# Optimization experiments

Measured on AMD Instinct MI355X. Metric: run time of the kernel, lower is better.

The kernel has to match this reference:

```python
import jax, jax.numpy as jnp
import numpy as np

MARGIN = 0.2
BIG = 1e9  # sentinel for masked (positive-pair) entries in the row-min


def setup_inputs() -> dict:
    key = jax.random.key(0)
    k1, k2, k3 = jax.random.split(key, 3)
    B, D, NUM_CLASSES = 4096, 512, 1000
    z_s = jax.random.normal(k1, (B, D), dtype=jnp.float32)
    z_i = jax.random.normal(k2, (B, D), dtype=jnp.float32)
    labels = jax.random.randint(k3, (B,), 0, NUM_CLASSES, dtype=jnp.int64)
    return {"z_s": z_s, "z_i": z_i, "labels": labels}


def reference(z_s, z_i, labels):
    # dists[a, b] = 1 - <z_s[a], z_i[b]>   -- [B, B]
    dists = 1.0 - jnp.einsum("ad,bd->ab", z_s, z_i)
    pos_mask = labels[:, None] == labels[None, :]  # [B, B] same-label pairs

    p = jnp.diagonal(dists)  # positive distance per anchor, [B]
    # hardest negative per anchor: min over entries with different label
    n = jnp.min(jnp.where(pos_mask, BIG, dists), axis=1)  # [B]
    has_neg = ~jnp.all(pos_mask, axis=1)  # anchors with at least one negative

    per_anchor = jax.nn.relu(p - n + MARGIN)  # [B]
    count = jnp.sum(has_neg)
    total = jnp.sum(jnp.where(has_neg, per_anchor, 0.0))
    # mean over anchors that had negatives; 0.0 if none (matches torch fallback)
    return jnp.where(count > 0, total / jnp.maximum(count, 1).astype(total.dtype), 0.0)
```

## Files before the change

### kernel.cpp

```cpp
#include <hip/hip_runtime.h>
#include <hip/hip_bf16.h>

typedef __attribute__((ext_vector_type(8))) short bf16x8;
typedef __attribute__((ext_vector_type(4))) float f32x4;

#define NB 4096
#define ND 512
#define MARGIN_F 0.2f

__device__ __forceinline__ unsigned int enc_f32(float f) {
    unsigned int b = __float_as_uint(f);
    return (b & 0x80000000u) ? ~b : (b | 0x80000000u);
}

__device__ __forceinline__ float dec_f32(unsigned int e) {
    unsigned int b = (e & 0x80000000u) ? (e & 0x7fffffffu) : ~e;
    return __uint_as_float(b);
}

__device__ __forceinline__ void gld_lds16(const void* g, void* l) {
    __builtin_amdgcn_global_load_lds((__attribute__((address_space(1))) void*)g,
                                     (__attribute__((address_space(3))) void*)l,
                                     16, 0, 0);
}

__device__ __forceinline__ float selv(f32x4 v, int r) {
    float s01 = (r & 1) ? v[1] : v[0];
    float s23 = (r & 1) ? v[3] : v[2];
    return (r & 2) ? s23 : s01;
}

__global__ __launch_bounds__(256) void k_prep(const float* __restrict__ zs,
                                              const float* __restrict__ zi,
                                              __hip_bfloat16* __restrict__ outb,
                                              unsigned int* __restrict__ rowmax) {
    const int bid = blockIdx.x;
    if (bid < 16) rowmax[bid * 256 + threadIdx.x] = 0u;

    int gid = bid * 256 + threadIdx.x;
    int mat = gid >> 18;
    int t   = gid & 0x3FFFF;
    int si  = t >> 6;
    int L   = t & 63;
    const float* src = mat ? zi : zs;
    int row = ((si >> 4) << 4) | (L & 15);
    int col = ((si & 15) << 5) | (((L >> 4) & 3) << 3);
    const float4* p = (const float4*)(src + (size_t)row * ND + col);
    float4 f0 = p[0];
    float4 f1 = p[1];
    union { __hip_bfloat16 h[8]; bf16x8 v; } u;
    u.h[0] = __float2bfloat16(f0.x);
    u.h[1] = __float2bfloat16(f0.y);
    u.h[2] = __float2bfloat16(f0.z);
    u.h[3] = __float2bfloat16(f0.w);
    u.h[4] = __float2bfloat16(f1.x);
    u.h[5] = __float2bfloat16(f1.y);
    u.h[6] = __float2bfloat16(f1.z);
    u.h[7] = __float2bfloat16(f1.w);
    bf16x8* dst = (bf16x8*)(outb + ((size_t)mat << 21) + ((size_t)si << 9) + (L << 3));
    *dst = u.v;
}

__global__ __launch_bounds__(512, 2) void k_gemm_rowmax(const __hip_bfloat16* __restrict__ zsb,
                                                        const __hip_bfloat16* __restrict__ zib,
                                                        const int* __restrict__ labels,
                                                        unsigned int* __restrict__ rowmax,
                                                        float* __restrict__ p_diag) {
    __shared__ __align__(16) unsigned char lds[131072];
    __shared__ int labA[256];
    __shared__ int labB[256];

    const int tid = threadIdx.x;
    const int bid = blockIdx.x;
    const int xcd = bid & 7, lid = bid >> 3;
    const int bx = ((xcd & 3) << 2) | (lid & 3);
    const int by = ((xcd >> 2) << 3) | (lid >> 2);

    if (tid < 256) labA[tid] = labels[by * 256 + tid];
    else           labB[tid & 255] = labels[bx * 256 + (tid & 255)];

    const char* gA = (const char*)zsb;
    const char* gB = (const char*)zib;
    const int inner = (tid & 127) << 4;
    const int aB16 = by * 16 + (tid >> 7);
    const int bB16 = bx * 16 + (tid >> 7);

#define STAGE(kt, h) do {                                                          \
        const char* _g = ((h) & 2) ? gB : gA;                                      \
        int _rb = (((h) & 2) ? bB16 : aB16) + (((h) & 1) << 3);                    \
        unsigned _ld = (((kt) & 1) << 16) + ((h) << 14) + (tid << 4);              \
        gld_lds16(_g + (((size_t)_rb) << 14) + ((kt) << 11) + inner, lds + _ld);   \
        gld_lds16(_g + (((size_t)(_rb + 4)) << 14) + ((kt) << 11) + inner,         \
                  lds + _ld + 8192);                                               \
    } while (0)

    const int w = tid >> 6, lane = tid & 63;
    const int w_m = w >> 2, w_n = w & 3;
    const unsigned fragOff = (unsigned)(lane << 4);
    const unsigned aBase = (unsigned)(w_m << 14) + fragOff;
    const unsigned bBase = 32768u + (unsigned)((w_n >> 1) << 14)
                         + (unsigned)(((w_n & 1) << 2) << 11) + fragOff;

    const f32x4 Z4 = (f32x4){0.f, 0.f, 0.f, 0.f};
    f32x4 acc00=Z4, acc01=Z4, acc02=Z4, acc03=Z4;
    f32x4 acc10=Z4, acc11=Z4, acc12=Z4, acc13=Z4;
    f32x4 acc20=Z4, acc21=Z4, acc22=Z4, acc23=Z4;
    f32x4 acc30=Z4, acc31=Z4, acc32=Z4, acc33=Z4;
    f32x4 acc40=Z4, acc41=Z4, acc42=Z4, acc43=Z4;
    f32x4 acc50=Z4, acc51=Z4, acc52=Z4, acc53=Z4;
    f32x4 acc60=Z4, acc61=Z4, acc62=Z4, acc63=Z4;
    f32x4 acc70=Z4, acc71=Z4, acc72=Z4, acc73=Z4;
    bf16x8 a_0, a_1, a_2, a_3, b_0, b_1, b_2, b_3;

#define MF(A, B, C) __builtin_amdgcn_mfma_f32_16x16x32_bf16((A), (B), (C), 0, 0, 0)
#define LDB(koff)                                                              \
    b_0 = *(const bf16x8*)(lds + par + bBase + (0 << 11) + (koff));            \
    b_1 = *(const bf16x8*)(lds + par + bBase + (1 << 11) + (koff));            \
    b_2 = *(const bf16x8*)(lds + par + bBase + (2 << 11) + (koff));            \
    b_3 = *(const bf16x8*)(lds + par + bBase + (3 << 11) + (koff));
#define LDA(mh, koff)                                                          \
    a_0 = *(const bf16x8*)(lds + par + aBase + ((((mh) << 2) + 0) << 11) + (koff)); \
    a_1 = *(const bf16x8*)(lds + par + aBase + ((((mh) << 2) + 1) << 11) + (koff)); \
    a_2 = *(const bf16x8*)(lds + par + aBase + ((((mh) << 2) + 2) << 11) + (koff)); \
    a_3 = *(const bf16x8*)(lds + par + aBase + ((((mh) << 2) + 3) << 11) + (koff));
#define ROW4(A, R)                                                             \
    acc##R##0 = MF((A), b_0, acc##R##0);                                       \
    acc##R##1 = MF((A), b_1, acc##R##1);                                       \
    acc##R##2 = MF((A), b_2, acc##R##2);                                       \
    acc##R##3 = MF((A), b_3, acc##R##3);
#define PHASE_SYNC()                                                           \
    __builtin_amdgcn_s_barrier();                                              \
    asm volatile("s_waitcnt lgkmcnt(0)" ::: "memory");                         \
    __builtin_amdgcn_sched_barrier(0);

    STAGE(0, 0); STAGE(0, 1); STAGE(0, 2); STAGE(0, 3);
    STAGE(1, 2); STAGE(1, 3);
    __syncthreads();

#pragma unroll
    for (int kt = 0; kt < 8; ++kt) {
        const unsigned par = (unsigned)((kt & 1) << 16);

        LDB(0)
        LDA(0, 0)
        if (kt < 7) STAGE(kt + 1, 0);
        PHASE_SYNC()
        __builtin_amdgcn_s_setprio(1);
        ROW4(a_0, 0) ROW4(a_1, 1) ROW4(a_2, 2) ROW4(a_3, 3)
        __builtin_amdgcn_s_setprio(0);
        __builtin_amdgcn_s_barrier();

        LDA(1, 0)
        if (kt < 7) STAGE(kt + 1, 1);
        PHASE_SYNC()
        __builtin_amdgcn_s_setprio(1);
        ROW4(a_0, 4) ROW4(a_1, 5) ROW4(a_2, 6) ROW4(a_3, 7)
        __builtin_amdgcn_s_setprio(0);
        __builtin_amdgcn_s_barrier();

        LDB(1024)
        LDA(0, 1024)
        PHASE_SYNC()
        __builtin_amdgcn_s_setprio(1);
        ROW4(a_0, 0) ROW4(a_1, 1) ROW4(a_2, 2) ROW4(a_3, 3)
        __builtin_amdgcn_s_setprio(0);
        __builtin_amdgcn_s_barrier();

        LDA(1, 1024)
        if (kt < 6) { STAGE(kt + 2, 2); STAGE(kt + 2, 3); }
        PHASE_SYNC()
        __builtin_amdgcn_s_setprio(1);
        ROW4(a_0, 4) ROW4(a_1, 5) ROW4(a_2, 6) ROW4(a_3, 7)
        __builtin_amdgcn_s_setprio(0);
        if (kt < 6) {
            asm volatile("s_waitcnt vmcnt(4)" ::: "memory");
            __builtin_amdgcn_s_barrier();
        } else if (kt == 6) {
            asm volatile("s_waitcnt vmcnt(0)" ::: "memory");
            __builtin_amdgcn_s_barrier();
        }
    }
#undef STAGE
#undef LDA
#undef LDB
#undef ROW4
#undef PHASE_SYNC

    const int quad = lane >> 4;
    const int lcol = lane & 15;
    const int epiBase = by * 256 + w_m * 128 + quad * 4;

    const int lb_0 = labB[w_n * 64 + 0 * 16 + lcol];
    const int lb_1 = labB[w_n * 64 + 1 * 16 + lcol];
    const int lb_2 = labB[w_n * 64 + 2 * 16 + lcol];
    const int lb_3 = labB[w_n * 64 + 3 * 16 + lcol];

#define EPIV(m, n, LB) {                                                       \
        float v0 = acc##m##n[0], v1 = acc##m##n[1];                            \
        float v2 = acc##m##n[2], v3 = acc##m##n[3];                            \
        if (la0 != (LB) && v0 > mx0) mx0 = v0;                                 \
        if (la1 != (LB) && v1 > mx1) mx1 = v1;                                 \
        if (la2 != (LB) && v2 > mx2) mx2 = v2;                                 \
        if (la3 != (LB) && v3 > mx3) mx3 = v3; }
#define EPIRED(m, r, MX) {                                                     \
        float mm = (MX);                                                       \
        mm = fmaxf(mm, __shfl_xor(mm, 1));                                     \
        mm = fmaxf(mm, __shfl_xor(mm, 2));                                     \
        mm = fmaxf(mm, __shfl_xor(mm, 4));                                     \
        mm = fmaxf(mm, __shfl_xor(mm, 8));                                     \
        if (lcol == 0 && mm > -2.9e38f)                                        \
            atomicMax(&rowmax[epiBase + (m) * 16 + (r)], enc_f32(mm)); }
#define EPIMS(m) {                                                             \
        int la0 = labA[w_m * 128 + (m) * 16 + quad * 4 + 0];                   \
        int la1 = labA[w_m * 128 + (m) * 16 + quad * 4 + 1];                   \
        int la2 = labA[w_m * 128 + (m) * 16 + quad * 4 + 2];                   \
        int la3 = labA[w_m * 128 + (m) * 16 + quad * 4 + 3];                   \
        float mx0 = -3.0e38f, mx1 = -3.0e38f, mx2 = -3.0e38f, mx3 = -3.0e38f;  \
        EPIV(m, 0, lb_0) EPIV(m, 1, lb_1) EPIV(m, 2, lb_2) EPIV(m, 3, lb_3)    \
        EPIRED(m, 0, mx0) EPIRED(m, 1, mx1) EPIRED(m, 2, mx2) EPIRED(m, 3, mx3) }

    EPIMS(0) EPIMS(1) EPIMS(2) EPIMS(3)
    EPIMS(4) EPIMS(5) EPIMS(6) EPIMS(7)
#undef EPIMS
#undef EPIRED
#undef EPIV

    if (bx == by && (w_n >> 1) == w_m && (lcol >> 2) == quad) {
        int r = lcol & 3;
        f32x4 d0 = (w_n & 1) ? acc40 : acc00;
        f32x4 d1 = (w_n & 1) ? acc51 : acc11;
        f32x4 d2 = (w_n & 1) ? acc62 : acc22;
        f32x4 d3 = (w_n & 1) ? acc73 : acc33;
        int base = by * 256 + w_m * 128 + ((w_n & 1) << 6) + lcol;
        p_diag[base +  0] = 1.0f - selv(d0, r);
        p_diag[base + 16] = 1.0f - selv(d1, r);
        p_diag[base + 32] = 1.0f - selv(d2, r);
        p_diag[base + 48] = 1.0f - selv(d3, r);
    }
}

__global__ __launch_bounds__(1024) void k_finalize(const unsigned int* __restrict__ rowmax,
                                                   const float* __restrict__ p_diag,
                                                   float* __restrict__ out) {
    int tid = threadIdx.x;
    float sum = 0.0f;
    int cnt = 0;
#pragma unroll
    for (int it = 0; it < 4; ++it) {
        int a = tid + it * 1024;
        unsigned int e = rowmax[a];
        if (e != 0u) {
            float n = 1.0f - dec_f32(e);
            float per = p_diag[a] - n + MARGIN_F;
            if (per > 0.0f) sum += per;
            cnt++;
        }
    }
#pragma unroll
    for (int off = 32; off > 0; off >>= 1) {
        sum += __shfl_xor(sum, off);
        cnt += __shfl_xor(cnt, off);
    }
    __shared__ float sSum[16];
    __shared__ int sCnt[16];
    int w = tid >> 6, lane = tid & 63;
    if (lane == 0) { sSum[w] = sum; sCnt[w] = cnt; }
    __syncthreads();
    if (tid == 0) {
        float ts = 0.0f;
        int tc = 0;
#pragma unroll
        for (int i = 0; i < 16; ++i) { ts += sSum[i]; tc += sCnt[i]; }
        out[0] = (tc > 0) ? ts / (float)tc : 0.0f;
    }
}

extern "C" void kernel_launch(void* const* d_in, const int* in_sizes, int n_in,
                              void* d_out, int out_size, void* d_ws, size_t ws_size,
                              hipStream_t stream) {
    (void)in_sizes; (void)n_in; (void)out_size; (void)ws_size;
    const float* zs = (const float*)d_in[0];
    const float* zi = (const float*)d_in[1];
    const int* labels = (const int*)d_in[2];
    float* out = (float*)d_out;

    char* ws = (char*)d_ws;
    __hip_bfloat16* zb = (__hip_bfloat16*)ws;
    unsigned int* rowmax = (unsigned int*)(ws + (8u << 20));
    float* p_diag = (float*)(ws + (8u << 20) + 16384);

    k_prep<<<2048, 256, 0, stream>>>(zs, zi, zb, rowmax);
    k_gemm_rowmax<<<256, 512, 0, stream>>>(zb, zb + (size_t)NB * ND, labels, rowmax, p_diag);
    k_finalize<<<1, 1024, 0, stream>>>(rowmax, p_diag, out);
}
```

Measured before the change: 97.80 us.

## Restructure LDS staging into k-half quarters with per-phase A/B loads

Changes the global-to-LDS staging so each stage loads both A and B for a half k-slice (1 KB columns per row) instead of splitting A and B loads across phases, and adjusts the LDS fragment addressing to match the new layout. The prefetch schedule now issues the next k-tile's two halves in the first and third phases, with vmcnt waits inserted after the second and fourth phases. The goal is to even out the memory traffic across the compute phases and shorten the prologue. The trade-off is that the wait points and dependencies change, which can expose load latency if the prefetch distance is now shorter.

```diff
diff --git a/kernel.cpp b/kernel.cpp
--- a/kernel.cpp
+++ b/kernel.cpp
@@ -77,29 +77,29 @@
     const int by = ((xcd >> 2) << 3) | (lid >> 2);
 
     if (tid < 256) labA[tid] = labels[by * 256 + tid];
-    else           labB[tid & 255] = labels[bx * 256 + (tid & 255)];
+    else           labB[tid & 255] = labels[bx * 256 + (tid - 256)];
 
     const char* gA = (const char*)zsb;
     const char* gB = (const char*)zib;
-    const int inner = (tid & 127) << 4;
-    const int aB16 = by * 16 + (tid >> 7);
-    const int bB16 = bx * 16 + (tid >> 7);
-
-#define STAGE(kt, h) do {                                                          \
-        const char* _g = ((h) & 2) ? gB : gA;                                      \
-        int _rb = (((h) & 2) ? bB16 : aB16) + (((h) & 1) << 3);                    \
-        unsigned _ld = (((kt) & 1) << 16) + ((h) << 14) + (tid << 4);              \
-        gld_lds16(_g + (((size_t)_rb) << 14) + ((kt) << 11) + inner, lds + _ld);   \
-        gld_lds16(_g + (((size_t)(_rb + 4)) << 14) + ((kt) << 11) + inner,         \
-                  lds + _ld + 8192);                                               \
+    const int rbw = tid >> 6;
+    const int cw  = (tid & 63) << 4;
+    const int aQ = by * 16;
+    const int bQ = bx * 16;
+
+#define STAGEQ(kt, q) do {                                                         \
+        size_t _gc = ((size_t)((((kt) << 1) | (q)) << 10)) + cw;                   \
+        unsigned _ld = (((kt) & 1) << 16) + ((q) << 14) + (tid << 4);              \
+        gld_lds16(gA + (((size_t)(aQ + rbw))     << 14) + _gc, lds + _ld);         \
+        gld_lds16(gA + (((size_t)(aQ + 8 + rbw)) << 14) + _gc, lds + _ld + 8192);  \
+        gld_lds16(gB + (((size_t)(bQ + rbw))     << 14) + _gc, lds + _ld + 32768); \
+        gld_lds16(gB + (((size_t)(bQ + 8 + rbw)) << 14) + _gc, lds + _ld + 40960); \
     } while (0)
 
     const int w = tid >> 6, lane = tid & 63;
     const int w_m = w >> 2, w_n = w & 3;
     const unsigned fragOff = (unsigned)(lane << 4);
-    const unsigned aBase = (unsigned)(w_m << 14) + fragOff;
-    const unsigned bBase = 32768u + (unsigned)((w_n >> 1) << 14)
-                         + (unsigned)(((w_n & 1) << 2) << 11) + fragOff;
+    const unsigned aBase2 = (unsigned)(w_m << 13) + fragOff;
+    const unsigned bBase2 = 32768u + (unsigned)(w_n << 12) + fragOff;
 
     const f32x4 Z4 = (f32x4){0.f, 0.f, 0.f, 0.f};
     f32x4 acc00=Z4, acc01=Z4, acc02=Z4, acc03=Z4;
@@ -113,16 +113,16 @@
     bf16x8 a_0, a_1, a_2, a_3, b_0, b_1, b_2, b_3;
 
 #define MF(A, B, C) __builtin_amdgcn_mfma_f32_16x16x32_bf16((A), (B), (C), 0, 0, 0)
-#define LDB(koff)                                                              \
-    b_0 = *(const bf16x8*)(lds + par + bBase + (0 << 11) + (koff));            \
-    b_1 = *(const bf16x8*)(lds + par + bBase + (1 << 11) + (koff));            \
-    b_2 = *(const bf16x8*)(lds + par + bBase + (2 << 11) + (koff));            \
-    b_3 = *(const bf16x8*)(lds + par + bBase + (3 << 11) + (koff));
-#define LDA(mh, koff)                                                          \
-    a_0 = *(const bf16x8*)(lds + par + aBase + ((((mh) << 2) + 0) << 11) + (koff)); \
-    a_1 = *(const bf16x8*)(lds + par + aBase + ((((mh) << 2) + 1) << 11) + (koff)); \
-    a_2 = *(const bf16x8*)(lds + par + aBase + ((((mh) << 2) + 2) << 11) + (koff)); \
-    a_3 = *(const bf16x8*)(lds + par + aBase + ((((mh) << 2) + 3) << 11) + (koff));
+#define LDBq(q)                                                                     \
+    b_0 = *(const bf16x8*)(lds + par + ((q) << 14) + bBase2 + (0 << 10));           \
+    b_1 = *(const bf16x8*)(lds + par + ((q) << 14) + bBase2 + (1 << 10));           \
+    b_2 = *(const bf16x8*)(lds + par + ((q) << 14) + bBase2 + (2 << 10));           \
+    b_3 = *(const bf16x8*)(lds + par + ((q) << 14) + bBase2 + (3 << 10));
+#define LDAq(mh, q)                                                                 \
+    a_0 = *(const bf16x8*)(lds + par + ((q) << 14) + aBase2 + ((((mh) << 2) + 0) << 10)); \
+    a_1 = *(const bf16x8*)(lds + par + ((q) << 14) + aBase2 + ((((mh) << 2) + 1) << 10)); \
+    a_2 = *(const bf16x8*)(lds + par + ((q) << 14) + aBase2 + ((((mh) << 2) + 2) << 10)); \
+    a_3 = *(const bf16x8*)(lds + par + ((q) << 14) + aBase2 + ((((mh) << 2) + 3) << 10));
 #define ROW4(A, R)                                                             \
     acc##R##0 = MF((A), b_0, acc##R##0);                                       \
     acc##R##1 = MF((A), b_1, acc##R##1);                                       \
@@ -133,56 +133,51 @@
     asm volatile("s_waitcnt lgkmcnt(0)" ::: "memory");                         \
     __builtin_amdgcn_sched_barrier(0);
 
-    STAGE(0, 0); STAGE(0, 1); STAGE(0, 2); STAGE(0, 3);
-    STAGE(1, 2); STAGE(1, 3);
+    STAGEQ(0, 0); STAGEQ(0, 1);
     __syncthreads();
 
 #pragma unroll
     for (int kt = 0; kt < 8; ++kt) {
         const unsigned par = (unsigned)((kt & 1) << 16);
 
-        LDB(0)
-        LDA(0, 0)
-        if (kt < 7) STAGE(kt + 1, 0);
+        LDBq(0)
+        LDAq(0, 0)
+        if (kt < 7) STAGEQ(kt + 1, 0);
         PHASE_SYNC()
         __builtin_amdgcn_s_setprio(1);
         ROW4(a_0, 0) ROW4(a_1, 1) ROW4(a_2, 2) ROW4(a_3, 3)
         __builtin_amdgcn_s_setprio(0);
         __builtin_amdgcn_s_barrier();
 
-        LDA(1, 0)
-        if (kt < 7) STAGE(kt + 1, 1);
+        LDAq(1, 0)
         PHASE_SYNC()
         __builtin_amdgcn_s_setprio(1);
         ROW4(a_0, 4) ROW4(a_1, 5) ROW4(a_2, 6) ROW4(a_3, 7)
         __builtin_amdgcn_s_setprio(0);
-        __builtin_amdgcn_s_barrier();
-
-        LDB(1024)
-        LDA(0, 1024)
+        if (kt < 7) asm volatile("s_waitcnt vmcnt(4)" ::: "memory");
+        else        asm volatile("s_waitcnt vmcnt(0)" ::: "memory");
+        __builtin_amdgcn_s_barrier();
+
+        LDBq(1)
+        LDAq(0, 1)
+        if (kt < 7) STAGEQ(kt + 1, 1);
         PHASE_SYNC()
         __builtin_amdgcn_s_setprio(1);
         ROW4(a_0, 0) ROW4(a_1, 1) ROW4(a_2, 2) ROW4(a_3, 3)
         __builtin_amdgcn_s_setprio(0);
         __builtin_amdgcn_s_barrier();
 
-        LDA(1, 1024)
-        if (kt < 6) { STAGE(kt + 2, 2); STAGE(kt + 2, 3); }
+        LDAq(1, 1)
         PHASE_SYNC()
         __builtin_amdgcn_s_setprio(1);
         ROW4(a_0, 4) ROW4(a_1, 5) ROW4(a_2, 6) ROW4(a_3, 7)
         __builtin_amdgcn_s_setprio(0);
-        if (kt < 6) {
-            asm volatile("s_waitcnt vmcnt(4)" ::: "memory");
-            __builtin_amdgcn_s_barrier();
-        } else if (kt == 6) {
-            asm volatile("s_waitcnt vmcnt(0)" ::: "memory");
-            __builtin_amdgcn_s_barrier();
-        }
-    }
-#undef STAGE
-#undef LDA
-#undef LDB
+        if (kt < 7) asm volatile("s_waitcnt vmcnt(4)" ::: "memory");
+        __builtin_amdgcn_s_barrier();
+    }
+#undef STAGEQ
+#undef LDAq
+#undef LDBq
 #undef ROW4
 #undef PHASE_SYNC
 
@@ -290,6 +285,7 @@
     float* p_diag = (float*)(ws + (8u << 20) + 16384);
 
     k_prep<<<2048, 256, 0, stream>>>(zs, zi, zb, rowmax);
-    k_gemm_rowmax<<<256, 512, 0, stream>>>(zb, zb + (size_t)NB * ND, labels, rowmax, p_diag);
+    dim3 g(256);
+    k_gemm_rowmax<<<g, 512, 0, stream>>>(zb, zb + (size_t)NB * ND, labels, rowmax, p_diag);
     k_finalize<<<1, 1024, 0, stream>>>(rowmax, p_diag, out);
 }
```

Result: no change. 99.48 us (+1.7%).
